# Optimization experiments

Measured on AMD Instinct MI355X. Metric: run time of the kernel, lower is better.

## Reference

```python
import jax, jax.numpy as jnp
import numpy as np

B, L, P = 65536, 512, 96
E_LIN, E = 14, 16
FFT = 512
TEMP = 0.07
K = 2
EPS = 1e-5


def setup_inputs() -> dict:
    key = jax.random.key(0)
    k0, k1, k2 = jax.random.split(key, 3)
    x = jax.random.normal(k0, (B, L), dtype=jnp.float32)
    Wg = jax.random.normal(k1, (E, FFT // 2), dtype=jnp.float32) * 0.02
    bg = jnp.zeros((E,), dtype=jnp.float32)
    Wr = jax.random.normal(k2, (E_LIN, P, L), dtype=jnp.float32) * 0.02
    br = jnp.zeros((E_LIN, P), dtype=jnp.float32)
    return {"x": x, "Wg": Wg, "bg": bg, "Wr": Wr, "br": br}


def _periodogram(x):
    # x: [B, L] -> normalized power spectrum [B, FFT//2]
    x0 = x - jnp.mean(x, axis=1, keepdims=True)
    dft = jnp.fft.fft(x0, n=FFT, axis=1) / np.float32(np.sqrt(FFT))
    dft = dft[:, : FFT // 2]
    I = dft.real ** 2 + dft.imag ** 2
    s = jnp.sum(I, axis=1, keepdims=True)
    s = jnp.where(s == 0, jnp.ones_like(s), s)
    return I / s


def reference(x, Wg, bg, Wr, br):
    # gating (eval mode: no noise, divide by temperature)
    I = _periodogram(x)                                  # [B, F/2]
    gate = (I @ Wg.T + bg) / TEMP                        # [B, E]
    topv, topi = jax.lax.top_k(gate, K)                  # [B, K]
    gates = jax.nn.softmax(topv, axis=1)                 # [B, K]

    # RLinear experts: RevIN(norm) -> Linear -> RevIN(denorm); stats detached
    mu = jax.lax.stop_gradient(jnp.mean(x, axis=1, keepdims=True))        # [B,1]
    sd = jax.lax.stop_gradient(jnp.sqrt(jnp.var(x, axis=1, keepdims=True) + EPS))
    xn = (x - mu) / sd                                   # [B, L]
    yr = jnp.einsum('bl,epl->bep', xn, Wr) + br          # [B, E_LIN, P]
    yr = yr * sd[:, :, None] + mu[:, :, None]

    mean_out = jnp.broadcast_to(jnp.mean(x, axis=1, keepdims=True), (x.shape[0], P))[:, None, :]
    naive_out = jnp.broadcast_to(x[:, -1:], (x.shape[0], P))[:, None, :]

    eo = jnp.concatenate([yr, mean_out, naive_out], axis=1)   # [B, E, P]
    sel = jnp.take_along_axis(eo, topi[:, :, None], axis=1)   # [B, K, P]
    out = jnp.sum(gates[:, :, None] * sel, axis=1)            # [B, P]
    return out
```

## Files before the change

### kernel.cpp

```cpp
#include <hip/hip_runtime.h>
#include <math.h>

#define NB_B 65536
#define NL   512
#define NP   96
#define NE   16
#define NEL  14
#define NF   256
#define TEMP_INV (1.0f/0.07f)
#define TAU  1e-5f
#define PI_D 3.14159265358979323846
#define MAXCHK 1280

typedef __attribute__((ext_vector_type(8))) short bf16x8;
typedef __attribute__((ext_vector_type(4))) float f32x4;


#define WS_PCNT     0
#define WS_PTK      16384
#define WS_PBASE    32768
#define WS_FLAGCNT  33792
#define WS_NCHK     33824
#define WS_FLAG     33856
#define WS_SSUM     296000
#define WS_WGT      301376
#define WS_BGT      317760
#define WS_TWF      317824
#define WS_TWD      319872
#define WS_REC      328064
#define WS_HDR      590208
#define WS_RIDX     1638784
#define WS_WRB      1900928
#define WS_DESC     3473792

__device__ __forceinline__ unsigned short f2bf(float f) {
    unsigned u = __float_as_uint(f);
    unsigned r = (u + 0x7fffu + ((u >> 16) & 1u)) >> 16;
    return (unsigned short)r;
}

__global__ __launch_bounds__(256) void k_prep(
    const float* __restrict__ Wg, const float* __restrict__ bg,
    const float* __restrict__ Wr,
    float* __restrict__ Ssum, float* __restrict__ WgT, float* __restrict__ bgT,
    float2* __restrict__ twf, double2* __restrict__ twd,
    int* __restrict__ pcnt, int* __restrict__ flagcnt)
{
    int g = blockIdx.x * 256 + threadIdx.x;
    if (g < NEL * NP) {
        const float4* w = (const float4*)(Wr + (size_t)g * NL);
        float s = 0.f;
        for (int i = 0; i < NL / 4; i++) { float4 v = w[i]; s += v.x + v.y + v.z + v.w; }
        Ssum[g] = s;
    }
    if (g < NF * NE) {
        int f = g >> 4, e = g & 15;
        WgT[g] = Wg[e * NF + f] * TEMP_INV;
    }
    if (g < NF) {
        double a = -2.0 * PI_D * (double)g / 512.0;
        twf[g] = make_float2((float)cos(a), (float)sin(a));
    }
    if (g < 512) {
        double a = -2.0 * PI_D * (double)g / 512.0;
        twd[g] = make_double2(cos(a), sin(a));
    }
    if (g < 256) pcnt[g << 4] = 0;
    if (g < NE) bgT[g] = bg[g] * TEMP_INV;
    if (g == 300) *flagcnt = 0;
}

__global__ __launch_bounds__(256) void k_cvt(
    const float4* __restrict__ Wr, ushort4* __restrict__ Wrb)
{
    int g = blockIdx.x * 256 + threadIdx.x;
    ushort4 o = make_ushort4(0, 0, 0, 0);
    if (g < NEL * NP * NL / 4) {
        float4 v = Wr[g];
        o.x = f2bf(v.x); o.y = f2bf(v.y); o.z = f2bf(v.z); o.w = f2bf(v.w);
    }
    Wrb[g] = o;
}

__global__ __launch_bounds__(256) void k_gate(
    const float* __restrict__ x,
    const float* __restrict__ WgT, const float* __restrict__ bgT,
    const float2* __restrict__ twf,
    int* __restrict__ rec, float4* __restrict__ hdr,
    int* __restrict__ flaglist, int* __restrict__ flagcnt)
{
    __shared__ float2 s_tw[256];
    __shared__ float2 s_z[4][576];
    __shared__ float  s_g[4][2][16];
    float* s_Iv = (float*)&s_z[0][0];

    const int t = threadIdx.x;
    const int wv = t >> 6, l = t & 63;
    const int b0 = blockIdx.x * 8 + wv * 2;
    s_tw[t] = twf[t];

    const float* xa = x + (size_t)b0 * NL;
    const float* xb = xa + NL;
    float xr[8], xi[8];
#pragma unroll
    for (int k = 0; k < 8; k++) { xr[k] = xa[k * 64 + l]; xi[k] = xb[k * 64 + l]; }

    float sa = 0.f, qa = 0.f, sb = 0.f, qb = 0.f;
#pragma unroll
    for (int k = 0; k < 8; k++) {
        sa += xr[k]; qa += xr[k] * xr[k];
        sb += xi[k]; qb += xi[k] * xi[k];
    }
#pragma unroll
    for (int m = 1; m < 64; m <<= 1) {
        sa += __shfl_xor(sa, m); qa += __shfl_xor(qa, m);
        sb += __shfl_xor(sb, m); qb += __shfl_xor(qb, m);
    }
    const float mu_a = sa * (1.f / 512.f);
    const float sd_a = sqrtf(qa * (1.f / 512.f) - mu_a * mu_a + 1e-5f);
    const float mu_b = sb * (1.f / 512.f);
    const float sd_b = sqrtf(qb * (1.f / 512.f) - mu_b * mu_b + 1e-5f);
    const float last_a = __shfl(xr[7], 63);
    const float last_b = __shfl(xi[7], 63);
#pragma unroll
    for (int k = 0; k < 8; k++) { xr[k] -= mu_a; xi[k] -= mu_b; }
    __syncthreads();

#pragma unroll
    for (int k = 0; k < 4; k++) {
        float2 w = s_tw[k * 64 + l];
        float ur = xr[k], ui = xi[k], vr = xr[k + 4], vi = xi[k + 4];
        xr[k] = ur + vr; xi[k] = ui + vi;
        float dr = ur - vr, di = ui - vi;
        xr[k + 4] = dr * w.x - di * w.y; xi[k + 4] = dr * w.y + di * w.x;
    }
    {
        const int kk[4] = {0, 1, 4, 5};
#pragma unroll
        for (int g2 = 0; g2 < 4; g2++) {
            int k = kk[g2];
            float2 w = s_tw[((k & 1) * 64 + l) << 1];
            float ur = xr[k], ui = xi[k], vr = xr[k + 2], vi = xi[k + 2];
            xr[k] = ur + vr; xi[k] = ui + vi;
            float dr = ur - vr, di = ui - vi;
            xr[k + 2] = dr * w.x - di * w.y; xi[k + 2] = dr * w.y + di * w.x;
        }
    }
    {
        float2 w = s_tw[l << 2];
#pragma unroll
        for (int k = 0; k < 8; k += 2) {
            float ur = xr[k], ui = xi[k], vr = xr[k + 1], vi = xi[k + 1];
            xr[k] = ur + vr; xi[k] = ui + vi;
            float dr = ur - vr, di = ui - vi;
            xr[k + 1] = dr * w.x - di * w.y; xi[k + 1] = dr * w.y + di * w.x;
        }
    }
#pragma unroll
    for (int st = 3; st < 9; st++) {
        const int half = 256 >> st;
        const int tt = (l & (half - 1)) << st;
        float2 w = s_tw[tt];
        const bool up = (l & half) != 0;
        const float cc = up ? w.x : 1.f;
        const float ss = up ? w.y : 0.f;
#pragma unroll
        for (int k = 0; k < 8; k++) {
            float pr = __shfl_xor(xr[k], half);
            float pi = __shfl_xor(xi[k], half);
            float ar = up ? (pr - xr[k]) : (xr[k] + pr);
            float ai = up ? (pi - xi[k]) : (xi[k] + pi);
            xr[k] = ar * cc - ai * ss;
            xi[k] = ar * ss + ai * cc;
        }
    }

#pragma unroll
    for (int k = 0; k < 8; k++) {
        int i = k * 64 + l;
        s_z[wv][i + (i >> 3)] = make_float2(xr[k], xi[k]);
    }
    __syncthreads();

    float Ia[4], Ib[4];
    float psa = 0.f, psb = 0.f;
#pragma unroll
    for (int j = 0; j < 4; j++) {
        int f = (l << 2) | j;
        int i1_ = (int)(__brev((unsigned)f) >> 23);
        int i2_ = (int)(__brev((unsigned)((512 - f) & 511)) >> 23);
        float2 z1 = s_z[wv][i1_ + (i1_ >> 3)];
        float2 z2 = s_z[wv][i2_ + (i2_ >> 3)];
        float pr_ = z1.x + z2.x, qm = z1.y - z2.y;
        float qp = z1.y + z2.y, pm = z1.x - z2.x;
        Ia[j] = pr_ * pr_ + qm * qm;
        Ib[j] = qp * qp + pm * pm;
        psa += Ia[j]; psb += Ib[j];
    }
#pragma unroll
    for (int m = 1; m < 64; m <<= 1) {
        psa += __shfl_xor(psa, m); psb += __shfl_xor(psb, m);
    }
    if (psa == 0.f) psa = 1.f;
    if (psb == 0.f) psb = 1.f;
    const float inv_a = 1.f / psa, inv_b = 1.f / psb;
    __syncthreads();

    float* myI = s_Iv + wv * 1152;
#pragma unroll
    for (int j = 0; j < 4; j++) {
        int f = (l << 2) | j;
        int fi = f + (f >> 3);
        myI[fi] = Ia[j];
        myI[288 + fi] = Ib[j];
    }
    __syncthreads();

    {
        int e = l >> 2, cq = l & 3;
        float acc_a = 0.f, acc_b = 0.f;
#pragma unroll 4
        for (int j = 0; j < 64; j++) {
            int f = cq * 64 + j;
            int fi = f + (f >> 3);
            float wgv = WgT[f * 16 + e];
            acc_a += myI[fi] * wgv;
            acc_b += myI[288 + fi] * wgv;
        }
        acc_a += __shfl_xor(acc_a, 1); acc_a += __shfl_xor(acc_a, 2);
        acc_b += __shfl_xor(acc_b, 1); acc_b += __shfl_xor(acc_b, 2);
        if (cq == 0) {
            s_g[wv][0][e] = acc_a * inv_a + bgT[e];
            s_g[wv][1][e] = acc_b * inv_b + bgT[e];
        }
    }
    __syncthreads();

#pragma unroll
    for (int r = 0; r < 2; r++) {
        if (l == 0) {
            const float mu = r ? mu_b : mu_a;
            const float sd = r ? sd_b : sd_a;
            const float last = r ? last_b : last_a;
            const int b = b0 + r;
            float b0v = -1e30f, b1v = -1e30f, b2v = -1e30f; int i0 = 0, i1 = 0;
            for (int i = 0; i < 16; i++) {
                float v = s_g[wv][r][i];
                if (v > b0v) { b2v = b1v; b1v = b0v; i1 = i0; b0v = v; i0 = i; }
                else if (v > b1v) { b2v = b1v; b1v = v; i1 = i; }
                else if (v > b2v) { b2v = v; }
            }
            float e1 = expf(b1v - b0v);
            float w0 = 1.f / (1.f + e1);
            rec[b] = i0 * 16 + i1;
            hdr[b] = make_float4(mu, sd, last, w0);
            if (b1v - b2v < TAU) {
                int pos = atomicAdd(flagcnt, 1);
                flaglist[pos] = b;
            }
        }
    }
}

__global__ __launch_bounds__(256) void k_refine(
    const float* __restrict__ x, const double2* __restrict__ twd,
    const float* __restrict__ Wg, const float* __restrict__ bg,
    int* __restrict__ rec, float4* __restrict__ hdr,
    const int* __restrict__ flaglist, const int* __restrict__ flagcnt)
{
    __shared__ double s_x[512];
    __shared__ double s_I[256];
    __shared__ double s_red[16];
    __shared__ double s_g[16];
    const int nf = *flagcnt;
    const int t = threadIdx.x;
    const int wid = t >> 6, lane = t & 63;
    for (int fi = blockIdx.x; fi < nf; fi += gridDim.x) {
        const int b = flaglist[fi];
        const float* xp = x + (size_t)b * NL;
        double v0 = (double)xp[t], v1 = (double)xp[t + 256];
        double lsum = v0 + v1;
        for (int m = 1; m < 64; m <<= 1) lsum += __shfl_xor(lsum, m);
        if (lane == 0) s_red[wid] = lsum;
        __syncthreads();
        double mu = (s_red[0] + s_red[1] + s_red[2] + s_red[3]) * (1.0 / 512.0);
        s_x[t] = v0 - mu; s_x[t + 256] = v1 - mu;
        __syncthreads();
        double2 w = twd[t];
        double pr = 1.0, pi = 0.0, cr = 0.0, ci = 0.0;
        for (int n = 0; n < 512; n++) {
            double xv = s_x[n];
            cr += xv * pr; ci += xv * pi;
            double t2 = pr * w.x - pi * w.y;
            pi = pr * w.y + pi * w.x;
            pr = t2;
        }
        double I = cr * cr + ci * ci;
        s_I[t] = I;
        double ls = I;
        for (int m = 1; m < 64; m <<= 1) ls += __shfl_xor(ls, m);
        if (lane == 0) s_red[8 + wid] = ls;
        __syncthreads();
        double stot = s_red[8] + s_red[9] + s_red[10] + s_red[11];
        if (stot == 0.0) stot = 1.0;
        if (t < 16) {
            double acc = 0.0;
            const float* wrow = Wg + t * NF;
            for (int f = 0; f < NF; f++) acc += s_I[f] * (double)wrow[f];
            s_g[t] = (acc / stot + (double)bg[t]) * (1.0 / 0.07);
        }
        __syncthreads();
        if (t == 0) {
            double c0 = -1e300, c1 = -1e300; int j0 = 0, j1 = 0;
            for (int i = 0; i < 16; i++) {
                double v = s_g[i];
                if (v > c0) { c1 = c0; j1 = j0; c0 = v; j0 = i; }
                else if (v > c1) { c1 = v; j1 = i; }
            }
            double e1 = exp(c1 - c0);
            float w0f = (float)(1.0 / (1.0 + e1));
            rec[b] = j0 * 16 + j1;
            ((float*)(hdr + b))[3] = w0f;
        }
        __syncthreads();
    }
}

__global__ __launch_bounds__(256) void k_count(
    const int* __restrict__ rec, int* __restrict__ pcnt)
{
    __shared__ int h[256];
    const int t = threadIdx.x;
    h[t] = 0;
    __syncthreads();
    atomicAdd(&h[rec[blockIdx.x * 256 + t]], 1);
    __syncthreads();
    if (h[t]) atomicAdd(&pcnt[t << 4], h[t]);
}

__global__ __launch_bounds__(256) void k_scan(
    const int* __restrict__ pcnt, int* __restrict__ pbase, int* __restrict__ ptk,
    int* __restrict__ desc, int* __restrict__ nchk)
{
    __shared__ int s[256], c[256];
    const int t = threadIdx.x;
    const int n = pcnt[t << 4];
    s[t] = n;
    c[t] = (n + 63) >> 6;
    __syncthreads();
    for (int off = 1; off < 256; off <<= 1) {
        int v1 = (t >= off) ? s[t - off] : 0;
        int v2 = (t >= off) ? c[t - off] : 0;
        __syncthreads();
        s[t] += v1; c[t] += v2;
        __syncthreads();
    }
    int excl = t ? s[t - 1] : 0;
    int cexcl = t ? c[t - 1] : 0;
    pbase[t] = excl;
    ptk[t << 4] = excl;
    int myc = (n + 63) >> 6;
    for (int j = 0; j < myc; j++) desc[cexcl + j] = (t << 16) | j;
    if (t == 255) *nchk = cexcl + myc;
}

__global__ __launch_bounds__(256) void k_scatter(
    const int* __restrict__ rec, int* __restrict__ ptk, int* __restrict__ ridx)
{
    __shared__ int h[256], base_[256];
    const int t = threadIdx.x;
    const int b = blockIdx.x * 256 + t;
    h[t] = 0;
    __syncthreads();
    int pid = rec[b];
    int lo = atomicAdd(&h[pid], 1);
    __syncthreads();
    if (h[t]) base_[t] = atomicAdd(&ptk[t << 4], h[t]);
    __syncthreads();
    ridx[base_[pid] + lo] = b;
}

__global__ __launch_bounds__(256) void k_gemm(
    const float* __restrict__ x, const unsigned short* __restrict__ Wrb,
    const float* __restrict__ br, const float* __restrict__ Ssum,
    const float4* __restrict__ hdr, float* __restrict__ out,
    const int* __restrict__ pcnt, const int* __restrict__ pbase,
    const int* __restrict__ ridx,
    const int* __restrict__ desc, const int* __restrict__ nchk)
{
    __shared__ __align__(16) unsigned short sA[64 * 72];
    __shared__ __align__(16) unsigned short sB[2][96 * 72];
    __shared__ int    s_idx[64];
    __shared__ float4 s_hdr[64];
    __shared__ float  s_br[2][96], s_S[2][96];
    if ((int)blockIdx.x >= *nchk) return;
    const int d = desc[blockIdx.x];
    const int pid = d >> 16, cc = d & 0xffff;
    const int n = pcnt[pid << 4];
    const int base = pbase[pid];
    const int i0 = pid >> 4, i1 = pid & 15;
    const int t = threadIdx.x;
    const int lane = t & 63, wv = t >> 6;
    const int quad = lane >> 4, l16 = lane & 15;
    const int ar = t >> 2, asub = t & 3;
    if (t < 96) {
        s_br[0][t] = (i0 < NEL) ? br[i0 * NP + t] : 0.f;
        s_S [0][t] = (i0 < NEL) ? Ssum[i0 * NP + t] : 0.f;
        s_br[1][t] = (i1 < NEL) ? br[i1 * NP + t] : 0.f;
        s_S [1][t] = (i1 < NEL) ? Ssum[i1 * NP + t] : 0.f;
    }
    if (t < 64) {
        int g = cc * 64 + t;
        bool vld = g < n;
        int row = vld ? ridx[base + g] : -1;
        s_idx[t] = row;
        s_hdr[t] = vld ? hdr[row] : make_float4(0.f, 0.f, 0.f, 0.f);
    }
    const unsigned short* wb0 = Wrb + (size_t)i0 * NP * NL;
    const unsigned short* wb1 = Wrb + (size_t)i1 * NP * NL;
    __syncthreads();

    f32x4 acc[2][6];
#pragma unroll
    for (int ex = 0; ex < 2; ex++)
#pragma unroll
        for (int j = 0; j < 6; j++) acc[ex][j] = (f32x4){0.f, 0.f, 0.f, 0.f};
    int rr = s_idx[ar]; if (rr < 0) rr = s_idx[0];
    const float* xrow = x + (size_t)rr * NL + asub * 16;

    for (int kb = 0; kb < NL; kb += 64) {
        {
            const float4* src = (const float4*)(xrow + kb);
            unsigned short tmp[16];
#pragma unroll
            for (int i = 0; i < 4; i++) {
                float4 v = src[i];
                tmp[i * 4 + 0] = f2bf(v.x); tmp[i * 4 + 1] = f2bf(v.y);
                tmp[i * 4 + 2] = f2bf(v.z); tmp[i * 4 + 3] = f2bf(v.w);
            }
            unsigned short* dst = sA + ar * 72 + asub * 16;
            *(bf16x8*)dst       = *(bf16x8*)tmp;
            *(bf16x8*)(dst + 8) = *(bf16x8*)(tmp + 8);
        }
#pragma unroll
        for (int it = 0; it < 6; it++) {
            int ex = (it >= 3);
            int fl = t + (it - 3 * ex) * 256;
            int p = fl >> 3, kg = fl & 7;
            const unsigned short* wb = ex ? wb1 : wb0;
            bf16x8 v = *(const bf16x8*)(wb + (size_t)p * NL + kb + kg * 8);
            *(bf16x8*)(&sB[ex][p * 72 + kg * 8]) = v;
        }
        __syncthreads();
#pragma unroll
        for (int ks = 0; ks < 2; ks++) {
            bf16x8 af = *(const bf16x8*)(sA + (wv * 16 + l16) * 72 + ks * 32 + quad * 8);
#pragma unroll
            for (int ex = 0; ex < 2; ex++)
#pragma unroll
                for (int nt = 0; nt < 6; nt++) {
                    bf16x8 bf = *(const bf16x8*)(&sB[ex][(nt * 16 + l16) * 72 + ks * 32 + quad * 8]);
                    acc[ex][nt] = __builtin_amdgcn_mfma_f32_16x16x32_bf16(af, bf, acc[ex][nt], 0, 0, 0);
                }
        }
        __syncthreads();
    }
#pragma unroll
    for (int i = 0; i < 4; i++) {
        int rloc = wv * 16 + quad * 4 + i;
        int row = s_idx[rloc];
        if (row >= 0) {
            float4 h = s_hdr[rloc];
            float mu = h.x, sd = h.y, last = h.z, w0 = h.w, w1 = 1.f - w0;
            float* orow = out + (size_t)row * NP;
#pragma unroll
            for (int nt = 0; nt < 6; nt++) {
                int p = nt * 16 + l16;
                float v0 = (i0 < NEL) ? (mu + s_br[0][p] * sd - mu * s_S[0][p] + acc[0][nt][i])
                                      : (i0 == NEL ? mu : last);
                float v1 = (i1 < NEL) ? (mu + s_br[1][p] * sd - mu * s_S[1][p] + acc[1][nt][i])
                                      : (i1 == NEL ? mu : last);
                orow[p] = w0 * v0 + w1 * v1;
            }
        }
    }
}

extern "C" void kernel_launch(void* const* d_in, const int* in_sizes, int n_in,
                              void* d_out, int out_size, void* d_ws, size_t ws_size,
                              hipStream_t stream)
{
    const float* x  = (const float*)d_in[0];
    const float* Wg = (const float*)d_in[1];
    const float* bg = (const float*)d_in[2];
    const float* Wr = (const float*)d_in[3];
    const float* br = (const float*)d_in[4];
    float* out = (float*)d_out;
    char* ws = (char*)d_ws;

    int*     pcnt     = (int*)(ws + WS_PCNT);
    int*     ptk      = (int*)(ws + WS_PTK);
    int*     pbase    = (int*)(ws + WS_PBASE);
    int*     flagcnt  = (int*)(ws + WS_FLAGCNT);
    int*     nchk     = (int*)(ws + WS_NCHK);
    int*     flaglist = (int*)(ws + WS_FLAG);
    float*   Ssum     = (float*)(ws + WS_SSUM);
    float*   WgT      = (float*)(ws + WS_WGT);
    float*   bgT      = (float*)(ws + WS_BGT);
    float2*  twf      = (float2*)(ws + WS_TWF);
    double2* twd      = (double2*)(ws + WS_TWD);
    int*     rec      = (int*)(ws + WS_REC);
    float4*  hdr      = (float4*)(ws + WS_HDR);
    int*     ridx     = (int*)(ws + WS_RIDX);
    unsigned short* Wrb = (unsigned short*)(ws + WS_WRB);
    int*     desc     = (int*)(ws + WS_DESC);

    k_prep<<<dim3(32), dim3(256), 0, stream>>>(Wg, bg, Wr, Ssum, WgT, bgT, twf, twd, pcnt, flagcnt);
    k_cvt<<<dim3(768), dim3(256), 0, stream>>>((const float4*)Wr, (ushort4*)Wrb);
    k_gate<<<dim3(NB_B / 8), dim3(256), 0, stream>>>(x, WgT, bgT, twf, rec, hdr,
                                                     flaglist, flagcnt);
    k_refine<<<dim3(512), dim3(256), 0, stream>>>(x, twd, Wg, bg, rec, hdr,
                                                  flaglist, flagcnt);
    k_count<<<dim3(NB_B / 256), dim3(256), 0, stream>>>(rec, pcnt);
    k_scan<<<dim3(1), dim3(256), 0, stream>>>(pcnt, pbase, ptk, desc, nchk);
    k_scatter<<<dim3(NB_B / 256), dim3(256), 0, stream>>>(rec, ptk, ridx);
    k_gemm<<<dim3(MAXCHK), dim3(256), 0, stream>>>(x, Wrb, br, Ssum, hdr, out,
                                                   pcnt, pbase, ridx, desc, nchk);
}
```

Baseline: 355.8 us.

## Fuse prep kernels, compute stats from FFT bins, warp-level top-k, fold counting into gate

Merges the bf16 weight conversion into the prep kernel and moves pair counting into the gate kernel via global atomics, with the refine kernel adjusting counts. The gate kernel no longer computes mean and variance directly. It derives the mean from the DC bin and the variance from the spectrum sum plus the Nyquist term (Parseval), and zeroes the DC bin instead of subtracting the mean. It also drops several block barriers, uses a float4 gating weight layout, and replaces the single-lane top-3 scan with shuffle reductions. This removes two launches and some reductions, but adds atomic contention on pcnt and a small risk of numerical differences in the statistics.

```diff
diff --git a/kernel.cpp b/kernel.cpp
--- a/kernel.cpp
+++ b/kernel.cpp
@@ -42,20 +42,29 @@
 __global__ __launch_bounds__(256) void k_prep(
     const float* __restrict__ Wg, const float* __restrict__ bg,
     const float* __restrict__ Wr,
-    float* __restrict__ Ssum, float* __restrict__ WgT, float* __restrict__ bgT,
+    float* __restrict__ Ssum, float* __restrict__ WgE, float* __restrict__ bgT,
     float2* __restrict__ twf, double2* __restrict__ twd,
-    int* __restrict__ pcnt, int* __restrict__ flagcnt)
+    int* __restrict__ pcnt, int* __restrict__ flagcnt,
+    ushort4* __restrict__ Wrb)
 {
     int g = blockIdx.x * 256 + threadIdx.x;
+    {
+        ushort4 o = make_ushort4(0, 0, 0, 0);
+        if (g < NEL * NP * NL / 4) {
+            float4 v = ((const float4*)Wr)[g];
+            o.x = f2bf(v.x); o.y = f2bf(v.y); o.z = f2bf(v.z); o.w = f2bf(v.w);
+        }
+        Wrb[g] = o;
+    }
     if (g < NEL * NP) {
         const float4* w = (const float4*)(Wr + (size_t)g * NL);
         float s = 0.f;
         for (int i = 0; i < NL / 4; i++) { float4 v = w[i]; s += v.x + v.y + v.z + v.w; }
         Ssum[g] = s;
     }
-    if (g < NF * NE) {
-        int f = g >> 4, e = g & 15;
-        WgT[g] = Wg[e * NF + f] * TEMP_INV;
+    if (g < 4096) {
+        int c = g & 3, e = (g >> 2) & 15, f4 = g >> 6;
+        WgE[g] = Wg[e * NF + f4 * 4 + c] * TEMP_INV;
     }
     if (g < NF) {
         double a = -2.0 * PI_D * (double)g / 512.0;
@@ -70,28 +79,16 @@
     if (g == 300) *flagcnt = 0;
 }
 
-__global__ __launch_bounds__(256) void k_cvt(
-    const float4* __restrict__ Wr, ushort4* __restrict__ Wrb)
-{
-    int g = blockIdx.x * 256 + threadIdx.x;
-    ushort4 o = make_ushort4(0, 0, 0, 0);
-    if (g < NEL * NP * NL / 4) {
-        float4 v = Wr[g];
-        o.x = f2bf(v.x); o.y = f2bf(v.y); o.z = f2bf(v.z); o.w = f2bf(v.w);
-    }
-    Wrb[g] = o;
-}
-
 __global__ __launch_bounds__(256) void k_gate(
     const float* __restrict__ x,
-    const float* __restrict__ WgT, const float* __restrict__ bgT,
+    const float4* __restrict__ WgE4, const float* __restrict__ bgT,
     const float2* __restrict__ twf,
     int* __restrict__ rec, float4* __restrict__ hdr,
-    int* __restrict__ flaglist, int* __restrict__ flagcnt)
+    int* __restrict__ flaglist, int* __restrict__ flagcnt,
+    int* __restrict__ pcnt)
 {
     __shared__ float2 s_tw[256];
-    __shared__ float2 s_z[4][576];
-    __shared__ float  s_g[4][2][16];
+    __shared__ __align__(16) float2 s_z[4][576];
     float* s_Iv = (float*)&s_z[0][0];
 
     const int t = threadIdx.x;
@@ -104,26 +101,8 @@
     float xr[8], xi[8];
 #pragma unroll
     for (int k = 0; k < 8; k++) { xr[k] = xa[k * 64 + l]; xi[k] = xb[k * 64 + l]; }
-
-    float sa = 0.f, qa = 0.f, sb = 0.f, qb = 0.f;
-#pragma unroll
-    for (int k = 0; k < 8; k++) {
-        sa += xr[k]; qa += xr[k] * xr[k];
-        sb += xi[k]; qb += xi[k] * xi[k];
-    }
-#pragma unroll
-    for (int m = 1; m < 64; m <<= 1) {
-        sa += __shfl_xor(sa, m); qa += __shfl_xor(qa, m);
-        sb += __shfl_xor(sb, m); qb += __shfl_xor(qb, m);
-    }
-    const float mu_a = sa * (1.f / 512.f);
-    const float sd_a = sqrtf(qa * (1.f / 512.f) - mu_a * mu_a + 1e-5f);
-    const float mu_b = sb * (1.f / 512.f);
-    const float sd_b = sqrtf(qb * (1.f / 512.f) - mu_b * mu_b + 1e-5f);
     const float last_a = __shfl(xr[7], 63);
     const float last_b = __shfl(xi[7], 63);
-#pragma unroll
-    for (int k = 0; k < 8; k++) { xr[k] -= mu_a; xi[k] -= mu_b; }
     __syncthreads();
 
 #pragma unroll
@@ -162,16 +141,17 @@
         const int tt = (l & (half - 1)) << st;
         float2 w = s_tw[tt];
         const bool up = (l & half) != 0;
+        const float sg = up ? -1.f : 1.f;
         const float cc = up ? w.x : 1.f;
         const float ss = up ? w.y : 0.f;
 #pragma unroll
         for (int k = 0; k < 8; k++) {
             float pr = __shfl_xor(xr[k], half);
             float pi = __shfl_xor(xi[k], half);
-            float ar = up ? (pr - xr[k]) : (xr[k] + pr);
-            float ai = up ? (pi - xi[k]) : (xi[k] + pi);
-            xr[k] = ar * cc - ai * ss;
-            xi[k] = ar * ss + ai * cc;
+            float tr = fmaf(sg, xr[k], pr);
+            float ti = fmaf(sg, xi[k], pi);
+            xr[k] = tr * cc - ti * ss;
+            xi[k] = tr * ss + ti * cc;
         }
     }
 
@@ -180,7 +160,6 @@
         int i = k * 64 + l;
         s_z[wv][i + (i >> 3)] = make_float2(xr[k], xi[k]);
     }
-    __syncthreads();
 
     float Ia[4], Ib[4];
     float psa = 0.f, psb = 0.f;
@@ -193,71 +172,84 @@
         float2 z2 = s_z[wv][i2_ + (i2_ >> 3)];
         float pr_ = z1.x + z2.x, qm = z1.y - z2.y;
         float qp = z1.y + z2.y, pm = z1.x - z2.x;
-        Ia[j] = pr_ * pr_ + qm * qm;
-        Ib[j] = qp * qp + pm * pm;
-        psa += Ia[j]; psb += Ib[j];
+        float va = pr_ * pr_ + qm * qm;
+        float vb = qp * qp + pm * pm;
+        if (f == 0) { va = 0.f; vb = 0.f; }
+        Ia[j] = va; Ib[j] = vb;
+        psa += va; psb += vb;
     }
 #pragma unroll
     for (int m = 1; m < 64; m <<= 1) {
         psa += __shfl_xor(psa, m); psb += __shfl_xor(psb, m);
     }
+    const float psa_raw = psa, psb_raw = psb;
     if (psa == 0.f) psa = 1.f;
     if (psb == 0.f) psb = 1.f;
     const float inv_a = 1.f / psa, inv_b = 1.f / psb;
-    __syncthreads();
-
-    float* myI = s_Iv + wv * 1152;
-#pragma unroll
-    for (int j = 0; j < 4; j++) {
-        int f = (l << 2) | j;
-        int fi = f + (f >> 3);
-        myI[fi] = Ia[j];
-        myI[288 + fi] = Ib[j];
-    }
-    __syncthreads();
-
-    {
-        int e = l >> 2, cq = l & 3;
-        float acc_a = 0.f, acc_b = 0.f;
+
+    const float2 Z0   = s_z[wv][0];
+    const float2 Z256 = s_z[wv][1];
+
+    float* wI = s_Iv + wv * 1152;
+    const int io = (l << 2) + ((l >> 4) << 2);
+    *(float4*)(wI + io)       = make_float4(Ia[0], Ia[1], Ia[2], Ia[3]);
+    *(float4*)(wI + 272 + io) = make_float4(Ib[0], Ib[1], Ib[2], Ib[3]);
+
+    const int e16 = l & 15, cq = l >> 4;
+    const float bgv = bgT[e16];
+    float accA = 0.f, accB = 0.f;
+    const float* rA = wI + cq * 68;
+    const float* rB = rA + 272;
 #pragma unroll 4
-        for (int j = 0; j < 64; j++) {
-            int f = cq * 64 + j;
-            int fi = f + (f >> 3);
-            float wgv = WgT[f * 16 + e];
-            acc_a += myI[fi] * wgv;
-            acc_b += myI[288 + fi] * wgv;
-        }
-        acc_a += __shfl_xor(acc_a, 1); acc_a += __shfl_xor(acc_a, 2);
-        acc_b += __shfl_xor(acc_b, 1); acc_b += __shfl_xor(acc_b, 2);
-        if (cq == 0) {
-            s_g[wv][0][e] = acc_a * inv_a + bgT[e];
-            s_g[wv][1][e] = acc_b * inv_b + bgT[e];
-        }
-    }
-    __syncthreads();
-
-#pragma unroll
-    for (int r = 0; r < 2; r++) {
-        if (l == 0) {
-            const float mu = r ? mu_b : mu_a;
-            const float sd = r ? sd_b : sd_a;
-            const float last = r ? last_b : last_a;
-            const int b = b0 + r;
-            float b0v = -1e30f, b1v = -1e30f, b2v = -1e30f; int i0 = 0, i1 = 0;
-            for (int i = 0; i < 16; i++) {
-                float v = s_g[wv][r][i];
-                if (v > b0v) { b2v = b1v; b1v = b0v; i1 = i0; b0v = v; i0 = i; }
-                else if (v > b1v) { b2v = b1v; b1v = v; i1 = i; }
-                else if (v > b2v) { b2v = v; }
-            }
-            float e1 = expf(b1v - b0v);
-            float w0 = 1.f / (1.f + e1);
-            rec[b] = i0 * 16 + i1;
-            hdr[b] = make_float4(mu, sd, last, w0);
-            if (b1v - b2v < TAU) {
-                int pos = atomicAdd(flagcnt, 1);
-                flaglist[pos] = b;
-            }
+    for (int jj = 0; jj < 16; jj++) {
+        float4 ia = *(const float4*)(rA + 4 * jj);
+        float4 ib = *(const float4*)(rB + 4 * jj);
+        float4 w = WgE4[(cq * 16 + jj) * 16 + e16];
+        accA += ia.x * w.x + ia.y * w.y + ia.z * w.z + ia.w * w.w;
+        accB += ib.x * w.x + ib.y * w.y + ib.z * w.z + ib.w * w.w;
+    }
+    accA += __shfl_xor(accA, 16); accA += __shfl_xor(accA, 32);
+    accB += __shfl_xor(accB, 16); accB += __shfl_xor(accB, 32);
+
+    float v = ((l & 16) ? accB * inv_b : accA * inv_a) + bgv;
+
+    float b0v = v; int b0i = e16;
+#pragma unroll
+    for (int m = 1; m < 16; m <<= 1) {
+        float ov = __shfl_xor(b0v, m); int oi = __shfl_xor(b0i, m);
+        if (ov > b0v || (ov == b0v && oi < b0i)) { b0v = ov; b0i = oi; }
+    }
+    float v1 = (e16 == b0i) ? -1e30f : v;
+    float b1v = v1; int b1i = e16;
+#pragma unroll
+    for (int m = 1; m < 16; m <<= 1) {
+        float ov = __shfl_xor(b1v, m); int oi = __shfl_xor(b1i, m);
+        if (ov > b1v || (ov == b1v && oi < b1i)) { b1v = ov; b1i = oi; }
+    }
+    float v2 = (e16 == b1i) ? -1e30f : v1;
+    float b2v = v2;
+#pragma unroll
+    for (int m = 1; m < 16; m <<= 1) {
+        float ov = __shfl_xor(b2v, m);
+        b2v = fmaxf(b2v, ov);
+    }
+
+    if (l == 0 || l == 16) {
+        const int r = l >> 4;
+        const int b = b0 + r;
+        const float mu = (r ? Z0.y : Z0.x) * (1.f / 512.f);
+        const float Jv = r ? Z256.y : Z256.x;
+        const float ps = r ? psb_raw : psa_raw;
+        const float sd = sqrtf((0.5f * ps + Jv * Jv) * (1.f / 262144.f) + 1e-5f);
+        const float last = r ? last_b : last_a;
+        const float w0 = 1.f / (1.f + expf(b1v - b0v));
+        const int pid = b0i * 16 + b1i;
+        rec[b] = pid;
+        hdr[b] = make_float4(mu, sd, last, w0);
+        atomicAdd(&pcnt[pid << 4], 1);
+        if (b1v - b2v < TAU) {
+            int pos = atomicAdd(flagcnt, 1);
+            flaglist[pos] = b;
         }
     }
 }
@@ -266,7 +258,8 @@
     const float* __restrict__ x, const double2* __restrict__ twd,
     const float* __restrict__ Wg, const float* __restrict__ bg,
     int* __restrict__ rec, float4* __restrict__ hdr,
-    const int* __restrict__ flaglist, const int* __restrict__ flagcnt)
+    const int* __restrict__ flaglist, const int* __restrict__ flagcnt,
+    int* __restrict__ pcnt)
 {
     __shared__ double s_x[512];
     __shared__ double s_I[256];
@@ -319,23 +312,17 @@
             }
             double e1 = exp(c1 - c0);
             float w0f = (float)(1.0 / (1.0 + e1));
-            rec[b] = j0 * 16 + j1;
+            int newpid = j0 * 16 + j1;
+            int old = rec[b];
+            if (newpid != old) {
+                atomicSub(&pcnt[old << 4], 1);
+                atomicAdd(&pcnt[newpid << 4], 1);
+                rec[b] = newpid;
+            }
             ((float*)(hdr + b))[3] = w0f;
         }
         __syncthreads();
     }
-}
-
-__global__ __launch_bounds__(256) void k_count(
-    const int* __restrict__ rec, int* __restrict__ pcnt)
-{
-    __shared__ int h[256];
-    const int t = threadIdx.x;
-    h[t] = 0;
-    __syncthreads();
-    atomicAdd(&h[rec[blockIdx.x * 256 + t]], 1);
-    __syncthreads();
-    if (h[t]) atomicAdd(&pcnt[t << 4], h[t]);
 }
 
 __global__ __launch_bounds__(256) void k_scan(
@@ -505,7 +492,7 @@
     int*     nchk     = (int*)(ws + WS_NCHK);
     int*     flaglist = (int*)(ws + WS_FLAG);
     float*   Ssum     = (float*)(ws + WS_SSUM);
-    float*   WgT      = (float*)(ws + WS_WGT);
+    float*   WgE      = (float*)(ws + WS_WGT);
     float*   bgT      = (float*)(ws + WS_BGT);
     float2*  twf      = (float2*)(ws + WS_TWF);
     double2* twd      = (double2*)(ws + WS_TWD);
@@ -515,13 +502,12 @@
     unsigned short* Wrb = (unsigned short*)(ws + WS_WRB);
     int*     desc     = (int*)(ws + WS_DESC);
 
-    k_prep<<<dim3(32), dim3(256), 0, stream>>>(Wg, bg, Wr, Ssum, WgT, bgT, twf, twd, pcnt, flagcnt);
-    k_cvt<<<dim3(768), dim3(256), 0, stream>>>((const float4*)Wr, (ushort4*)Wrb);
-    k_gate<<<dim3(NB_B / 8), dim3(256), 0, stream>>>(x, WgT, bgT, twf, rec, hdr,
-                                                     flaglist, flagcnt);
+    k_prep<<<dim3(768), dim3(256), 0, stream>>>(Wg, bg, Wr, Ssum, WgE, bgT, twf, twd,
+                                                pcnt, flagcnt, (ushort4*)Wrb);
+    k_gate<<<dim3(NB_B / 8), dim3(256), 0, stream>>>(x, (const float4*)WgE, bgT, twf,
+                                                     rec, hdr, flaglist, flagcnt, pcnt);
     k_refine<<<dim3(512), dim3(256), 0, stream>>>(x, twd, Wg, bg, rec, hdr,
-                                                  flaglist, flagcnt);
-    k_count<<<dim3(NB_B / 256), dim3(256), 0, stream>>>(rec, pcnt);
+                                                  flaglist, flagcnt, pcnt);
     k_scan<<<dim3(1), dim3(256), 0, stream>>>(pcnt, pbase, ptk, desc, nchk);
     k_scatter<<<dim3(NB_B / 256), dim3(256), 0, stream>>>(rec, ptk, ridx);
     k_gemm<<<dim3(MAXCHK), dim3(256), 0, stream>>>(x, Wrb, br, Ssum, hdr, out,
```

Result: faster. 320.7 us (-9.9%).
